# Kernel tuning notes

Hardware: AMD Instinct MI355X
Metric: run time of the kernel (lower is better)

Reference implementation:

```python
import jax, jax.numpy as jnp
import numpy as np

NUM_NODE = 100000
B, L, D = 128, 50, 128
HOP = 2
S = 8            # n_sample
NEIGHBOR_N = 9   # FindNeighbors top-k
BETA = 0.005
LEAKY = 0.2      # opt.alpha


def _local_agg(h, adj, a_local):
    # h: [B,N,D], adj: [B,N,N] int with edge types 0..4, a_local: [4,D]
    # e_k[b,i,j] = leakyrelu(sum_d h[b,i,d]*h[b,j,d]*a_k[d]) without [B,N,N,D] blowup
    e = jnp.stack([jnp.einsum('bid,bjd->bij', h * a_local[k], h) for k in range(4)])
    e = jax.nn.leaky_relu(e, LEAKY)
    att = jnp.full(e.shape[1:], -9e15, dtype=h.dtype)
    for k in range(4):
        att = jnp.where(adj == k + 1, e[k], att)
    att = jax.nn.softmax(att, axis=-1)
    return att @ h


def _global_agg(self_v, neigh_v, neigh_w, extra, w1, w2, w3):
    # self_v [B,M,D], neigh_v [B,M,S,D], neigh_w [B,M,S], extra (session info) [B,M,D]
    x = jnp.concatenate([extra[:, :, None, :] * neigh_v, neigh_w[..., None]], axis=-1)  # [B,M,S,D+1]
    alpha = jax.nn.leaky_relu(jnp.einsum('bmse,ed->bmsd', x, w1), LEAKY)
    alpha = jax.nn.softmax(jnp.einsum('bmsd,d->bms', alpha, w2[:, 0]), axis=-1)
    neigh = jnp.sum(alpha[..., None] * neigh_v, axis=-2)                                # [B,M,D]
    out = jnp.concatenate([self_v, neigh], axis=-1) @ w3
    return jax.nn.relu(out)


def _ssl(h_local, h_global):
    b, l, _ = h_local.shape
    kr, kc = jax.random.split(jax.random.key(42))
    corrupted = h_local[jax.random.permutation(kr, b)][:, jax.random.permutation(kc, l)]
    pos = jnp.sum(h_local * h_global, axis=1)
    neg = jnp.sum(h_global * corrupted, axis=1)
    return jnp.sum(-jnp.log(1e-8 + jax.nn.sigmoid(pos))
                   - jnp.log(1e-8 + 1.0 - jax.nn.sigmoid(neg)))


def _compute_scores(hidden, mask, pos_embedding, w1, w2, glu1_w, glu1_b, glu2_w, embedding):
    b, l, d = hidden.shape
    m = mask.astype(hidden.dtype)[..., None]                       # [B,L,1]
    pos = jnp.broadcast_to(pos_embedding[:l][None], hidden.shape)  # [B,L,D]
    hs = jnp.sum(hidden * m, axis=1) / jnp.sum(m, axis=1)          # [B,D]
    nh = jnp.tanh(jnp.concatenate([pos, hidden], axis=-1) @ w1)
    ns = jax.nn.sigmoid(nh @ glu1_w.T + glu1_b + hs[:, None, :] @ glu2_w.T)
    beta = (ns @ w2) * m                                           # [B,L,1]
    select = jnp.sum(beta * hidden, axis=1)                        # [B,D]
    # FindNeighbors: top-k cosine-similarity attention across the batch
    norm = jnp.sqrt(jnp.sum(select * select + 1e-6, axis=1))[:, None]
    cos = jax.nn.softmax((select @ select.T) / (norm @ norm.T), axis=-1)
    k = min(NEIGHBOR_N, b)
    topv, topi = jax.lax.top_k(cos, k)
    topv = jax.nn.softmax(topv, axis=-1)
    neighbor = jnp.sum(topv[..., None] * select[topi], axis=1)     # [B,D]
    select = select + neighbor                                     # dropout40: eval identity
    return select @ embedding[1:].T                                # [B, num_node-1]


def _forward(inputs, adj, mask_item, item, adj_all, num_w, embedding, pos_embedding,
             a_local, gw1, gw2, gw3, w1, w2, glu1_w, glu1_b, glu2_w):
    b, l = inputs.shape
    d = embedding.shape[1]
    h = embedding[inputs]
    h_local = _local_agg(h, adj, a_local)
    # multi-hop neighbor sampling via global adjacency table
    item_neighbors = [inputs]
    weight_neighbors = []
    support = l
    for _ in range(HOP):
        flat = item_neighbors[-1].reshape(-1)
        support *= S
        item_neighbors.append(adj_all[flat].reshape(b, support))
        weight_neighbors.append(num_w[flat].reshape(b, support))
    entity = [embedding[x] for x in item_neighbors]
    mf = mask_item.astype(h.dtype)
    item_emb = embedding[item] * mf[..., None]
    sess = jnp.sum(item_emb, axis=1) / jnp.sum(mf, axis=-1)[:, None]   # [B,D]
    session_info = [jnp.broadcast_to(sess[:, None, :], ev.shape) for ev in entity[:HOP]]
    for n_hop in range(HOP):
        nxt = []
        for i in range(HOP - n_hop):
            nv = entity[i + 1].reshape(b, -1, S, d)
            nw = weight_neighbors[i].reshape(b, -1, S)
            nxt.append(_global_agg(entity[i], nv, nw, session_info[i],
                                   gw1[n_hop], gw2[n_hop], gw3[n_hop]))
        entity = nxt
    h_global = entity[0].reshape(b, l, d)
    output = h_local + h_global  # dropout_local/global: eval identity
    con_loss = _ssl(h_local, h_global)
    scores = _compute_scores(output, mask_item, pos_embedding, w1, w2,
                             glu1_w, glu1_b, glu2_w, embedding)
    return output, BETA * con_loss, scores


def setup_inputs() -> dict:
    key = jax.random.key(0)
    ks = jax.random.split(key, 18)
    s = 0.08  # ~ uniform(-1/sqrt(D), 1/sqrt(D)) scale
    return {
        'inputs': jax.random.randint(ks[0], (B, L), 0, NUM_NODE, dtype=jnp.int32),
        'adj': jax.random.randint(ks[1], (B, L, L), 0, 5, dtype=jnp.int32),
        'mask_item': jax.random.randint(ks[2], (B, L), 0, 2, dtype=jnp.int32).at[:, 0].set(1),
        'item': jax.random.randint(ks[3], (B, L), 0, NUM_NODE, dtype=jnp.int32),
        'targets': jax.random.randint(ks[4], (B,), 0, NUM_NODE, dtype=jnp.int32),
        'adj_all': jax.random.randint(ks[5], (NUM_NODE, S), 0, NUM_NODE, dtype=jnp.int32),
        'num_w': jax.random.uniform(ks[6], (NUM_NODE, S), dtype=jnp.float32),
        'embedding': jax.random.normal(ks[7], (NUM_NODE, D), dtype=jnp.float32) * s,
        'pos_embedding': jax.random.normal(ks[8], (200, D), dtype=jnp.float32) * s,
        'a_local': jax.random.normal(ks[9], (4, D), dtype=jnp.float32) * s,
        'gw1': jax.random.normal(ks[10], (HOP, D + 1, D), dtype=jnp.float32) * s,
        'gw2': jax.random.normal(ks[11], (HOP, D, 1), dtype=jnp.float32) * s,
        'gw3': jax.random.normal(ks[12], (HOP, 2 * D, D), dtype=jnp.float32) * s,
        'w1': jax.random.normal(ks[13], (2 * D, D), dtype=jnp.float32) * s,
        'w2': jax.random.normal(ks[14], (D, 1), dtype=jnp.float32) * s,
        'glu1_w': jax.random.normal(ks[15], (D, D), dtype=jnp.float32) * s,
        'glu1_b': jax.random.normal(ks[16], (D,), dtype=jnp.float32) * s,
        'glu2_w': jax.random.normal(ks[17], (D, D), dtype=jnp.float32) * s,
    }


def reference(inputs, adj, mask_item, item, targets, adj_all, num_w, embedding,
              pos_embedding, a_local, gw1, gw2, gw3, w1, w2, glu1_w, glu1_b, glu2_w):
    # targets embedding lookup in the original is dead code (targets1 unused)
    return _forward(inputs, adj, mask_item, item, adj_all, num_w, embedding,
                    pos_embedding, a_local, gw1, gw2, gw3, w1, w2, glu1_w, glu1_b, glu2_w)
```

## Files before the change

kernel.cpp:

```cpp
#include <hip/hip_runtime.h>
#include <stdint.h>

namespace {
constexpr int B_ = 128;
constexpr int L_ = 50;
constexpr int D_ = 128;
constexpr int S_ = 8;
constexpr int NSC_ = 99999;
constexpr int NBR_ = 9;
}
#define LEAKY_ 0.2f
#define BETA_ 0.005f

typedef __attribute__((ext_vector_type(8))) __bf16 bf16x8;
typedef __attribute__((ext_vector_type(4))) float f32x4;

__device__ __forceinline__ float leaky_(float x){ return x >= 0.f ? x : LEAKY_*x; }
__device__ __forceinline__ float sigm_(float x){ return 1.f/(1.f+expf(-x)); }

__device__ __forceinline__ short f2b(float f){
  uint32_t u = __float_as_uint(f);
  u += 0x7fffu + ((u >> 16) & 1u);
  return (short)(u >> 16);
}
__device__ __forceinline__ float b2f(short s){
  return __uint_as_float(((uint32_t)(uint16_t)s) << 16);
}
__device__ __forceinline__ f32x4 zero4(){ f32x4 z = {0.f,0.f,0.f,0.f}; return z; }
__device__ __forceinline__ f32x4 mfma_bf16(bf16x8 a, bf16x8 b, f32x4 c){
  return __builtin_amdgcn_mfma_f32_16x16x32_bf16(a, b, c, 0, 0, 0);
}

__device__ __forceinline__ void tf2x32(uint32_t k0, uint32_t k1, uint32_t c0, uint32_t c1,
                                       uint32_t* o0, uint32_t* o1){
  uint32_t ks2 = k0 ^ k1 ^ 0x1BD11BDAu;
  uint32_t x0 = c0 + k0, x1 = c1 + k1;
#define RND_(r) { x0 += x1; x1 = (x1<<(r))|(x1>>(32-(r))); x1 ^= x0; }
  RND_(13) RND_(15) RND_(26) RND_(6)   x0 += k1;  x1 += ks2 + 1u;
  RND_(17) RND_(29) RND_(16) RND_(24)  x0 += ks2; x1 += k0  + 2u;
  RND_(13) RND_(15) RND_(26) RND_(6)   x0 += k0;  x1 += k1  + 3u;
  RND_(17) RND_(29) RND_(16) RND_(24)  x0 += k1;  x1 += ks2 + 4u;
  RND_(13) RND_(15) RND_(26) RND_(6)   x0 += ks2; x1 += k0  + 5u;
#undef RND_
  *o0 = x0; *o1 = x1;
}

__global__ __launch_bounds__(256) void k_prep_all(
    const float* __restrict__ emb, const int* __restrict__ item,
    const int* __restrict__ mask, const float* __restrict__ gw1,
    const float* __restrict__ gw3, const float* __restrict__ glu1w,
    const int* __restrict__ inputs, const int* __restrict__ adj_all,
    const float* __restrict__ num_w,
    short* __restrict__ embB, float* __restrict__ glu1wT,
    short* __restrict__ w3T,
    int* __restrict__ n1i, float* __restrict__ n1w,
    int* __restrict__ n2i, float* __restrict__ n2w,
    short* __restrict__ Bsess)
{
  int blk = blockIdx.x, tid = threadIdx.x;
  if (blk < 3125){
    size_t base = (size_t)blk*4096 + (size_t)tid*16;
    float4 f0 = *(const float4*)(emb + base);
    float4 f1 = *(const float4*)(emb + base + 4);
    float4 f2 = *(const float4*)(emb + base + 8);
    float4 f3 = *(const float4*)(emb + base + 12);
    short4 s0, s1, s2, s3;
    s0.x=f2b(f0.x); s0.y=f2b(f0.y); s0.z=f2b(f0.z); s0.w=f2b(f0.w);
    s1.x=f2b(f1.x); s1.y=f2b(f1.y); s1.z=f2b(f1.z); s1.w=f2b(f1.w);
    s2.x=f2b(f2.x); s2.y=f2b(f2.y); s2.z=f2b(f2.z); s2.w=f2b(f2.w);
    s3.x=f2b(f3.x); s3.y=f2b(f3.y); s3.z=f2b(f3.z); s3.w=f2b(f3.w);
    *(short4*)(embB + base)      = s0;
    *(short4*)(embB + base + 4)  = s1;
    *(short4*)(embB + base + 8)  = s2;
    *(short4*)(embB + base + 12) = s3;
  } else if (blk < 3445){
    int o = (blk - 3125)*256 + tid;
    if (o < 16384){
      int e = o >> 7, t = o & 127;
      glu1wT[o] = glu1w[t*128 + e];
    } else {
      int o3 = o - 16384;
      int hop = o3 >> 15, r = o3 & 32767;
      int nn = r >> 8, k = r & 255;
      w3T[hop*(128*264) + nn*264 + k] = f2b(gw3[hop*(256*128) + k*128 + nn]);
    }
  } else if (blk < 3645){
    int p = (blk - 3445)*256 + tid;
    int base = inputs[p >> 3];
    int off  = base*S_ + (p & 7);
    int i1 = adj_all[off];
    n1i[p] = i1;
    n1w[p] = num_w[off];
#pragma unroll
    for (int j = 0; j < 8; j++){
      n2i[(size_t)p*8 + j] = adj_all[i1*8 + j];
      n2w[(size_t)p*8 + j] = num_w[i1*8 + j];
    }
  } else {
    int i = blk - 3645;
    int hop = i >> 7, b = i & 127;
    __shared__ float sessS[128];
    if (tid < 128){
      float acc = 0.f, ms = 0.f;
      for (int l = 0; l < L_; l++){
        float mk = (float)mask[b*L_ + l];
        ms += mk;
        acc += mk * emb[(size_t)item[b*L_ + l]*D_ + tid];
      }
      sessS[tid] = acc / ms;
    }
    __syncthreads();
    const float* g1 = gw1 + hop*(129*128);
    short* outp = Bsess + ((size_t)hop*128 + b)*16384;
    for (int it = 0; it < 64; it++){
      int u = it*256 + tid;
      int e = u & 127, d = u >> 7;
      outp[u] = f2b(g1[e*128 + d] * sessS[e]);
    }
  }
}

__global__ __launch_bounds__(256, 4) void k_fused1(
    const short* __restrict__ embB, const int* __restrict__ inputs,
    const int* __restrict__ adj, const float* __restrict__ a_local,
    float* __restrict__ hl,
    const int* __restrict__ n1i, const float* __restrict__ n1w,
    const int* __restrict__ n2i, const float* __restrict__ n2w,
    const short* __restrict__ Bsess,
    const float* __restrict__ w1g, const float* __restrict__ w2g,
    short* __restrict__ e0pB, short* __restrict__ e1pB)
{
  __shared__ __align__(16) short As[128*136];
  __shared__ float w1lS[128], w2S[128], nwsS[128], logitsS[128], alphaS[128];
  const int blk = blockIdx.x;
  const int tid = threadIdx.x;

  if (blk < 256){
    float* hs   = (float*)As;
    float* attL = (float*)(As + 12900);
    float* al   = (float*)(As + 15500);
    int*   idxs = (int*)  (As + 16556);
    int b = blk >> 1, half = blk & 1;
    int i0 = half*25;
    if (tid < L_) idxs[tid] = inputs[b*L_ + tid];
    __syncthreads();
    for (int u = tid; u < L_*16; u += 256){
      int i = u >> 4, c = u & 15;
      union { bf16x8 v; short sh[8]; } w;
      w.v = *(const bf16x8*)&embB[(size_t)idxs[i]*128 + c*8];
#pragma unroll
      for (int j = 0; j < 8; j++) hs[i*129 + c*8 + j] = b2f(w.sh[j]);
    }
    for (int e = tid; e < 4*D_; e += 256) al[(e>>7)*132 + (e&127)] = a_local[e];
    __syncthreads();
    for (int p = tid; p < 25*L_; p += 256){
      int il = p / L_, j = p % L_;
      int i = i0 + il;
      int k = adj[((size_t)b*L_ + i)*L_ + j];
      float v = -9e15f;
      if (k >= 1){
        const float* ak = &al[(k-1)*132];
        float acc = 0.f;
        for (int d = 0; d < D_; d++) acc += hs[i*129+d]*hs[j*129+d]*ak[d];
        v = leaky_(acc);
      }
      attL[il*52 + j] = v;
    }
    __syncthreads();
    if (tid < 25){
      int il = tid;
      float mx = -INFINITY;
      for (int j = 0; j < L_; j++) mx = fmaxf(mx, attL[il*52+j]);
      float sm = 0.f;
      for (int j = 0; j < L_; j++){ float e_ = expf(attL[il*52+j] - mx); attL[il*52+j] = e_; sm += e_; }
      float inv = 1.f/sm;
      for (int j = 0; j < L_; j++) attL[il*52+j] *= inv;
    }
    __syncthreads();
    for (int q = tid; q < 25*D_; q += 256){
      int il = q >> 7, d = q & 127;
      float acc = 0.f;
      for (int j = 0; j < L_; j++) acc += attL[il*52+j]*hs[j*129+d];
      hl[((size_t)b*L_ + i0 + il)*D_ + d] = acc;
    }
    return;
  }

  int b, r0, rpb;
  const int* nidx; const float* nw; short* outn;
  if (blk < 768){
    int i = blk - 256;
    b = i >> 2; r0 = (i & 3)*128;
    nidx = n1i; nw = n1w; outn = e0pB; rpb = 400;
  } else {
    int i = blk - 768;
    b = i / 25; r0 = (i % 25)*128;
    nidx = n2i; nw = n2w; outn = e1pB; rpb = 3200;
  }
  if (tid < 128){
    w1lS[tid]  = w1g[128*128 + tid];
    w2S[tid]   = w2g[tid];
    int rr = min(r0 + tid, rpb - 1);
    nwsS[tid]  = nw[(size_t)b*rpb + rr];
  }
  for (int it = 0; it < 8; it++){
    int u = it*256 + tid;
    int lr = u >> 4, c = u & 15;
    int rr = min(r0 + lr, rpb - 1);
    const short* src = embB + (size_t)nidx[(size_t)b*rpb + rr]*128;
    *(bf16x8*)&As[lr*136 + c*8] = *(const bf16x8*)&src[c*8];
  }
  __syncthreads();
  const int lane = tid & 63, wave = tid >> 6;
  const int quad = lane >> 4, l16 = lane & 15;
  const int wr0 = wave * 32;
  const short* Bb = Bsess + (size_t)b*16384;
  f32x4 acc[2][8];
#pragma unroll
  for (int i=0;i<2;i++)
#pragma unroll
    for (int j=0;j<8;j++) acc[i][j] = zero4();
  for (int kc = 0; kc < 4; kc++){
    int k = kc*32 + quad*8;
    bf16x8 a0 = *(const bf16x8*)&As[(wr0 + l16)*136 + k];
    bf16x8 a1 = *(const bf16x8*)&As[(wr0 + 16 + l16)*136 + k];
    bf16x8 bb[8];
#pragma unroll
    for (int nt = 0; nt < 8; nt++)
      bb[nt] = *(const bf16x8*)&Bb[(size_t)(nt*16 + l16)*128 + k];
#pragma unroll
    for (int nt = 0; nt < 8; nt++){
      acc[0][nt] = mfma_bf16(a0, bb[nt], acc[0][nt]);
      acc[1][nt] = mfma_bf16(a1, bb[nt], acc[1][nt]);
    }
  }
#pragma unroll
  for (int rt = 0; rt < 2; rt++){
#pragma unroll
    for (int r = 0; r < 4; r++){
      int rowl = wr0 + rt*16 + quad*4 + r;
      float nwv = nwsS[rowl];
      float c = 0.f;
#pragma unroll
      for (int nt = 0; nt < 8; nt++){
        int col = nt*16 + l16;
        float v = acc[rt][nt][r] + nwv * w1lS[col];
        c += leaky_(v) * w2S[col];
      }
      c += __shfl_xor(c, 1, 64);
      c += __shfl_xor(c, 2, 64);
      c += __shfl_xor(c, 4, 64);
      c += __shfl_xor(c, 8, 64);
      if (l16 == 0) logitsS[rowl] = c;
    }
  }
  __syncthreads();
  if (tid < 16){
    float mx = -INFINITY;
    for (int s = 0; s < 8; s++) mx = fmaxf(mx, logitsS[tid*8+s]);
    float sm = 0.f; float ev[8];
    for (int s = 0; s < 8; s++){ ev[s] = expf(logitsS[tid*8+s]-mx); sm += ev[s]; }
    for (int s = 0; s < 8; s++) alphaS[tid*8+s] = ev[s]/sm;
  }
  __syncthreads();
  {
    int mg = tid >> 4;
    int dc = tid & 15;
    float o[8];
#pragma unroll
    for (int j = 0; j < 8; j++) o[j] = 0.f;
#pragma unroll
    for (int s = 0; s < 8; s++){
      float al2 = alphaS[mg*8+s];
      union { bf16x8 v; short sh[8]; } u;
      u.v = *(const bf16x8*)&As[(mg*8+s)*136 + dc*8];
#pragma unroll
      for (int j = 0; j < 8; j++) o[j] += al2 * b2f(u.sh[j]);
    }
    if (r0 + mg*8 < rpb){
      int m = (r0 >> 3) + mg;
      union { short s[8]; bf16x8 v; } pk;
#pragma unroll
      for (int j = 0; j < 8; j++) pk.s[j] = f2b(o[j]);
      *(bf16x8*)(outn + ((size_t)b*(rpb>>3) + m)*128 + dc*8) = pk.v;
    }
  }
}

__global__ __launch_bounds__(256, 4) void k_att(
    const short* __restrict__ embB, const short* __restrict__ denseB,
    const int* __restrict__ nidx, const float* __restrict__ nw,
    const short* __restrict__ Bsess,
    const float* __restrict__ w1g, const float* __restrict__ w2g,
    short* __restrict__ outn, int rpb)
{
  __shared__ __align__(16) short As[128*136];
  __shared__ float w1lS[128], w2S[128], nwsS[128], logitsS[128], alphaS[128];
  const int tid = threadIdx.x;
  const int b = blockIdx.y;
  const int r0 = blockIdx.x * 128;
  if (tid < 128){
    w1lS[tid]  = w1g[128*128 + tid];
    w2S[tid]   = w2g[tid];
    int rr = min(r0 + tid, rpb - 1);
    nwsS[tid]  = nw[(size_t)b*rpb + rr];
  }
  for (int it = 0; it < 8; it++){
    int u = it*256 + tid;
    int lr = u >> 4, c = u & 15;
    int rr = min(r0 + lr, rpb - 1);
    const short* src = denseB ? denseB + ((size_t)b*rpb + rr)*128
                              : embB + (size_t)nidx[(size_t)b*rpb + rr]*128;
    *(bf16x8*)&As[lr*136 + c*8] = *(const bf16x8*)&src[c*8];
  }
  __syncthreads();
  const int lane = tid & 63, wave = tid >> 6;
  const int quad = lane >> 4, l16 = lane & 15;
  const int wr0 = wave * 32;
  const short* Bb = Bsess + (size_t)b*16384;
  f32x4 acc[2][8];
#pragma unroll
  for (int i=0;i<2;i++)
#pragma unroll
    for (int j=0;j<8;j++) acc[i][j] = zero4();
  for (int kc = 0; kc < 4; kc++){
    int k = kc*32 + quad*8;
    bf16x8 a0 = *(const bf16x8*)&As[(wr0 + l16)*136 + k];
    bf16x8 a1 = *(const bf16x8*)&As[(wr0 + 16 + l16)*136 + k];
    bf16x8 bb[8];
#pragma unroll
    for (int nt = 0; nt < 8; nt++)
      bb[nt] = *(const bf16x8*)&Bb[(size_t)(nt*16 + l16)*128 + k];
#pragma unroll
    for (int nt = 0; nt < 8; nt++){
      acc[0][nt] = mfma_bf16(a0, bb[nt], acc[0][nt]);
      acc[1][nt] = mfma_bf16(a1, bb[nt], acc[1][nt]);
    }
  }
#pragma unroll
  for (int rt = 0; rt < 2; rt++){
#pragma unroll
    for (int r = 0; r < 4; r++){
      int rowl = wr0 + rt*16 + quad*4 + r;
      float nwv = nwsS[rowl];
      float c = 0.f;
#pragma unroll
      for (int nt = 0; nt < 8; nt++){
        int col = nt*16 + l16;
        float v = acc[rt][nt][r] + nwv * w1lS[col];
        c += leaky_(v) * w2S[col];
      }
      c += __shfl_xor(c, 1, 64);
      c += __shfl_xor(c, 2, 64);
      c += __shfl_xor(c, 4, 64);
      c += __shfl_xor(c, 8, 64);
      if (l16 == 0) logitsS[rowl] = c;
    }
  }
  __syncthreads();
  if (tid < 16){
    float mx = -INFINITY;
    for (int s = 0; s < 8; s++) mx = fmaxf(mx, logitsS[tid*8+s]);
    float sm = 0.f; float ev[8];
    for (int s = 0; s < 8; s++){ ev[s] = expf(logitsS[tid*8+s]-mx); sm += ev[s]; }
    for (int s = 0; s < 8; s++) alphaS[tid*8+s] = ev[s]/sm;
  }
  __syncthreads();
  {
    int mg = tid >> 4;
    int dc = tid & 15;
    float o[8];
#pragma unroll
    for (int j = 0; j < 8; j++) o[j] = 0.f;
#pragma unroll
    for (int s = 0; s < 8; s++){
      float al = alphaS[mg*8+s];
      union { bf16x8 v; short sh[8]; } u;
      u.v = *(const bf16x8*)&As[(mg*8+s)*136 + dc*8];
#pragma unroll
      for (int j = 0; j < 8; j++) o[j] += al * b2f(u.sh[j]);
    }
    if (r0 + mg*8 < rpb){
      int m = (r0 >> 3) + mg;
      union { short s[8]; bf16x8 v; } pk;
#pragma unroll
      for (int j = 0; j < 8; j++) pk.s[j] = f2b(o[j]);
      *(bf16x8*)(outn + ((size_t)b*(rpb>>3) + m)*128 + dc*8) = pk.v;
    }
  }
}

__global__ __launch_bounds__(256) void k_gout2(
    const short* __restrict__ embB, const int* __restrict__ inputs,
    const int* __restrict__ n1i, const short* __restrict__ w3T,
    short* __restrict__ e0pB, short* __restrict__ e1pB)
{
  const int blk = blockIdx.x;
  const int* self_idx; short* buf; int rblk;
  if (blk < 100){ self_idx = inputs; buf = e0pB; rblk = blk; }
  else          { self_idx = n1i;    buf = e1pB; rblk = blk - 100; }
  const int tid = threadIdx.x;
  const int lane = tid & 63, wave = tid >> 6;
  const int quad = lane >> 4, l16 = lane & 15;
  const int rbase = rblk*64 + wave*16;
  const int row = rbase + l16;
  const short* selfp = embB + (size_t)self_idx[row]*128;
  const short* neighp = buf + (size_t)row*128;
  f32x4 acc[8];
#pragma unroll
  for (int i=0;i<8;i++) acc[i] = zero4();
  for (int kc = 0; kc < 4; kc++){
    int k = kc*32 + quad*8;
    bf16x8 a = *(const bf16x8*)&selfp[k];
#pragma unroll
    for (int nt = 0; nt < 8; nt++){
      bf16x8 bb = *(const bf16x8*)&w3T[(size_t)(nt*16 + l16)*264 + k];
      acc[nt] = mfma_bf16(a, bb, acc[nt]);
    }
  }
  for (int kc = 4; kc < 8; kc++){
    int k = kc*32 + quad*8;
    bf16x8 a = *(const bf16x8*)&neighp[k - 128];
#pragma unroll
    for (int nt = 0; nt < 8; nt++){
      bf16x8 bb = *(const bf16x8*)&w3T[(size_t)(nt*16 + l16)*264 + k];
      acc[nt] = mfma_bf16(a, bb, acc[nt]);
    }
  }
#pragma unroll
  for (int nt = 0; nt < 8; nt++)
#pragma unroll
    for (int r = 0; r < 4; r++){
      int orow = rbase + quad*4 + r;
      buf[(size_t)orow*128 + nt*16 + l16] = f2b(fmaxf(acc[nt][r], 0.f));
    }
}

__global__ __launch_bounds__(256) void k_gout(
    const short* __restrict__ embB, const short* __restrict__ selfB,
    const int* __restrict__ self_idx, const short* __restrict__ w3T,
    const short* __restrict__ neighB, float* __restrict__ outF,
    short* __restrict__ outB)
{
  const int tid = threadIdx.x;
  const int lane = tid & 63, wave = tid >> 6;
  const int quad = lane >> 4, l16 = lane & 15;
  const int rbase = blockIdx.x*64 + wave*16;
  const int row = rbase + l16;
  const short* selfp = self_idx ? embB + (size_t)self_idx[row]*128
                                : selfB + (size_t)row*128;
  const short* neighp = neighB + (size_t)row*128;
  f32x4 acc[8];
#pragma unroll
  for (int i=0;i<8;i++) acc[i] = zero4();
  for (int kc = 0; kc < 4; kc++){
    int k = kc*32 + quad*8;
    bf16x8 a = *(const bf16x8*)&selfp[k];
#pragma unroll
    for (int nt = 0; nt < 8; nt++){
      bf16x8 bb = *(const bf16x8*)&w3T[(size_t)(nt*16 + l16)*264 + k];
      acc[nt] = mfma_bf16(a, bb, acc[nt]);
    }
  }
  for (int kc = 4; kc < 8; kc++){
    int k = kc*32 + quad*8;
    bf16x8 a = *(const bf16x8*)&neighp[k - 128];
#pragma unroll
    for (int nt = 0; nt < 8; nt++){
      bf16x8 bb = *(const bf16x8*)&w3T[(size_t)(nt*16 + l16)*264 + k];
      acc[nt] = mfma_bf16(a, bb, acc[nt]);
    }
  }
  if (outF){
#pragma unroll
    for (int nt = 0; nt < 8; nt++)
#pragma unroll
      for (int r = 0; r < 4; r++){
        int orow = rbase + quad*4 + r;
        outF[(size_t)orow*128 + nt*16 + l16] = fmaxf(acc[nt][r], 0.f);
      }
  } else {
#pragma unroll
    for (int nt = 0; nt < 8; nt++)
#pragma unroll
      for (int r = 0; r < 4; r++){
        int orow = rbase + quad*4 + r;
        outB[(size_t)orow*128 + nt*16 + l16] = f2b(fmaxf(acc[nt][r], 0.f));
      }
  }
}

__global__ __launch_bounds__(128) void k_sslhs(
    const float* __restrict__ hl, const float* __restrict__ hg,
    const int* __restrict__ mask, const float* __restrict__ glu2_w,
    float* __restrict__ out, float* __restrict__ wsLoss,
    float* __restrict__ g2)
{
  __shared__ uint32_t keys[128];
  __shared__ float red[128];
  __shared__ float hss[128];
  __shared__ int pcS[50];
  __shared__ int prbS;
  int b = blockIdx.x, tid = threadIdx.x;
  uint32_t kr0, kr1, kc0, kc1, sk0, sk1, o0, o1;
  tf2x32(0u, 42u, 0u, 0u, &kr0, &kr1);
  tf2x32(0u, 42u, 0u, 1u, &kc0, &kc1);
  tf2x32(kr0, kr1, 0u, 1u, &sk0, &sk1);
  tf2x32(sk0, sk1, 0u, (uint32_t)tid, &o0, &o1);
  keys[tid] = o0 ^ o1;
  __syncthreads();
  {
    uint32_t mk = keys[tid];
    int rank = 0;
    for (int j = 0; j < 128; j++){
      uint32_t kj = keys[j];
      rank += (kj < mk) || (kj == mk && j < tid);
    }
    if (rank == b) prbS = tid;
  }
  __syncthreads();
  tf2x32(kc0, kc1, 0u, 1u, &sk0, &sk1);
  if (tid < 50){
    tf2x32(sk0, sk1, 0u, (uint32_t)tid, &o0, &o1);
    keys[tid] = o0 ^ o1;
  }
  __syncthreads();
  if (tid < 50){
    uint32_t mk = keys[tid];
    int rank = 0;
    for (int j = 0; j < 50; j++){
      uint32_t kj = keys[j];
      rank += (kj < mk) || (kj == mk && j < tid);
    }
    pcS[rank] = tid;
  }
  __syncthreads();
  int prb = prbS, d = tid;
  float pos = 0.f, neg = 0.f, hsacc = 0.f, ms = 0.f;
  for (int l = 0; l < L_; l++){
    size_t off = ((size_t)b*L_ + l)*D_ + d;
    float hlv = hl[off], hgv = hg[off];
    float o = hlv + hgv;
    out[off] = o;
    pos += hlv * hgv;
    neg += hgv * hl[((size_t)prb*L_ + pcS[l])*D_ + d];
    float mk = (float)mask[b*L_ + l];
    ms += mk;
    hsacc += mk * o;
  }
  hss[d] = hsacc / ms;
  red[d] = -logf(1e-8f + sigm_(pos)) - logf(1e-8f + 1.f - sigm_(neg));
  __syncthreads();
  for (int off = 64; off >= 1; off >>= 1){
    if (d < off) red[d] += red[d + off];
    __syncthreads();
  }
  if (d == 0) wsLoss[b] = red[0];
  float g = 0.f;
  for (int e = 0; e < 128; e++) g += hss[e]*glu2_w[d*128 + e];
  g2[(size_t)b*128 + d] = g;
}

__global__ __launch_bounds__(256) void k_beta10(
    const float* __restrict__ hidden, const int* __restrict__ mask,
    const float* __restrict__ pose, const float* __restrict__ w1s,
    const float* __restrict__ w2s, const float* __restrict__ glu1wT,
    const float* __restrict__ glu1b, const float* __restrict__ g2,
    float* __restrict__ betaW)
{
  __shared__ float x[10][260];
  __shared__ float buf[10][132];
  __shared__ float bufB[2][16];
  int lg = blockIdx.x, b = blockIdx.y, tid = threadIdx.x;
  int t = tid & 127, eh = tid >> 7;
  int l0 = lg*10;
  for (int u = tid; u < 10*64; u += 256){
    int row = u >> 6, c4 = u & 63;
    float4 v; int col;
    if (c4 < 32){ v = *(const float4*)(pose + (l0+row)*128 + c4*4); col = c4*4; }
    else        { v = *(const float4*)(hidden + ((size_t)b*L_ + l0+row)*128 + (c4-32)*4); col = 128 + (c4-32)*4; }
    *(float4*)&x[row][col] = v;
  }
  __syncthreads();
  float acc[10];
#pragma unroll
  for (int l = 0; l < 10; l++) acc[l] = 0.f;
  {
    int e0 = eh*128;
    for (int e = e0; e < e0 + 128; e += 4){
      float wa = w1s[(e+0)*128 + t];
      float wb = w1s[(e+1)*128 + t];
      float wc = w1s[(e+2)*128 + t];
      float wd = w1s[(e+3)*128 + t];
#pragma unroll
      for (int l = 0; l < 10; l++){
        float4 xv = *(const float4*)&x[l][e];
        acc[l] += xv.x*wa; acc[l] += xv.y*wb; acc[l] += xv.z*wc; acc[l] += xv.w*wd;
      }
    }
  }
  if (eh == 1){
#pragma unroll
    for (int i = 0; i < 10; i++) buf[i][t] = acc[i];
  }
  __syncthreads();
  if (eh == 0){
#pragma unroll
    for (int i = 0; i < 10; i++) acc[i] += buf[i][t];
  }
  __syncthreads();
  if (eh == 0){
#pragma unroll
    for (int l = 0; l < 10; l++) x[l][t] = tanhf(acc[l]);
  }
  __syncthreads();
  float acc2[10];
#pragma unroll
  for (int l = 0; l < 10; l++) acc2[l] = 0.f;
  {
    int e0 = eh*64;
    for (int e = e0; e < e0 + 64; e += 4){
      float wa = glu1wT[(e+0)*128 + t];
      float wb = glu1wT[(e+1)*128 + t];
      float wc = glu1wT[(e+2)*128 + t];
      float wd = glu1wT[(e+3)*128 + t];
#pragma unroll
      for (int l = 0; l < 10; l++){
        float4 xv = *(const float4*)&x[l][e];
        acc2[l] += xv.x*wa; acc2[l] += xv.y*wb; acc2[l] += xv.z*wc; acc2[l] += xv.w*wd;
      }
    }
  }
  if (eh == 1){
#pragma unroll
    for (int i = 0; i < 10; i++) buf[i][t] = acc2[i];
  }
  __syncthreads();
  if (eh == 0){
#pragma unroll
    for (int i = 0; i < 10; i++) acc2[i] += buf[i][t];
  }
  __syncthreads();
  if (eh == 0){
    float g2v = g2[(size_t)b*128 + t];
    float g1b = glu1b[t];
    float w2v = w2s[t];
    int lane = tid & 63, wv = tid >> 6;
#pragma unroll
    for (int l = 0; l < 10; l++){
      float ns = sigm_(acc2[l] + g1b + g2v);
      float v = ns * w2v;
      v += __shfl_xor(v, 1, 64);
      v += __shfl_xor(v, 2, 64);
      v += __shfl_xor(v, 4, 64);
      v += __shfl_xor(v, 8, 64);
      v += __shfl_xor(v, 16, 64);
      v += __shfl_xor(v, 32, 64);
      if (lane == 0) bufB[wv][l] = v;
    }
  }
  __syncthreads();
  if (tid < 10)
    betaW[b*L_ + l0 + tid] = (bufB[0][tid] + bufB[1][tid]) * (float)mask[b*L_ + l0 + tid];
}

__global__ __launch_bounds__(128) void k_selnorm(
    const float* __restrict__ hidden, const float* __restrict__ betaW,
    float* __restrict__ select, float* __restrict__ norms)
{
  __shared__ float bet[56];
  __shared__ float red[128];
  int b = blockIdx.x, t = threadIdx.x;
  if (t < L_) bet[t] = betaW[b*L_ + t];
  __syncthreads();
  float sel = 0.f;
  for (int l = 0; l < L_; l++) sel += bet[l]*hidden[((size_t)b*L_ + l)*128 + t];
  select[(size_t)b*128 + t] = sel;
  red[t] = sel*sel + 1e-6f;
  __syncthreads();
  for (int off=64; off>=1; off>>=1){ if (t<off) red[t]+=red[t+off]; __syncthreads(); }
  if (t==0) norms[b] = sqrtf(red[0]);
}

__global__ __launch_bounds__(128) void k_topk(const float* __restrict__ select,
                                              const float* __restrict__ norms,
                                              const float* __restrict__ wsLoss,
                                              short* __restrict__ select2b,
                                              float* __restrict__ out_loss){
  __shared__ float p[B_];
  __shared__ float red[128];
  __shared__ float tv[NBR_];
  __shared__ int   ti[NBR_];
  int b = blockIdx.x, t = threadIdx.x;
  float dot = 0.f;
  for (int d = 0; d < D_; d++) dot += select[(size_t)b*D_ + d]*select[(size_t)t*D_ + d];
  float logit = dot / (norms[b]*norms[t]);
  red[t] = logit; __syncthreads();
  for (int off = 64; off >= 1; off >>= 1){
    if (t < off) red[t] = fmaxf(red[t], red[t + off]);
    __syncthreads();
  }
  float mx = red[0]; __syncthreads();
  float e_ = expf(logit - mx);
  red[t] = e_; __syncthreads();
  for (int off = 64; off >= 1; off >>= 1){
    if (t < off) red[t] += red[t + off];
    __syncthreads();
  }
  p[t] = e_ / red[0];
  __syncthreads();
  if (t == 0){
    unsigned long long used0 = 0ull, used1 = 0ull;
    for (int k = 0; k < NBR_; k++){
      float best = -INFINITY; int bi = 0;
      for (int j = 0; j < B_; j++){
        bool u = (j < 64) ? ((used0 >> j) & 1ull) : ((used1 >> (j-64)) & 1ull);
        if (!u && p[j] > best){ best = p[j]; bi = j; }
      }
      if (bi < 64) used0 |= 1ull << bi; else used1 |= 1ull << (bi-64);
      tv[k] = best; ti[k] = bi;
    }
    float mx2 = -INFINITY;
    for (int k = 0; k < NBR_; k++) mx2 = fmaxf(mx2, tv[k]);
    float s2 = 0.f;
    for (int k = 0; k < NBR_; k++){ tv[k] = expf(tv[k]-mx2); s2 += tv[k]; }
    for (int k = 0; k < NBR_; k++) tv[k] /= s2;
  }
  __syncthreads();
  float nb = 0.f;
#pragma unroll
  for (int k = 0; k < NBR_; k++) nb += tv[k]*select[(size_t)ti[k]*D_ + t];
  select2b[(size_t)b*D_ + t] = f2b(select[(size_t)b*D_ + t] + nb);
  if (b == 0){
    __syncthreads();
    red[t] = wsLoss[t];
    __syncthreads();
    for (int off = 64; off >= 1; off >>= 1){
      if (t < off) red[t] += red[t + off];
      __syncthreads();
    }
    if (t == 0) out_loss[0] = BETA_ * red[0];
  }
}

__global__ __launch_bounds__(256) void k_scores(
    const short* __restrict__ sel2b, const float* __restrict__ emb,
    float* __restrict__ scores)
{
  __shared__ __align__(16) short Es[64*136];
  const int tid = threadIdx.x;
  const int n0 = blockIdx.x*64;
  for (int it = 0; it < 8; it++){
    int u = it*256 + tid;
    int lr = u >> 5, c = u & 31;
    int n = min(n0 + lr, NSC_ - 1);
    float4 v = *(const float4*)(emb + (size_t)(1 + n)*128 + c*4);
    short4 s4; s4.x=f2b(v.x); s4.y=f2b(v.y); s4.z=f2b(v.z); s4.w=f2b(v.w);
    *(short4*)&Es[lr*136 + c*4] = s4;
  }
  __syncthreads();
  const int lane = tid & 63, wave = tid >> 6;
  const int quad = lane >> 4, l16 = lane & 15;
  int n = n0 + wave*16 + l16;
  f32x4 acc[8];
#pragma unroll
  for (int i=0;i<8;i++) acc[i] = zero4();
  for (int kc = 0; kc < 4; kc++){
    int k = kc*32 + quad*8;
    bf16x8 bb = *(const bf16x8*)&Es[(wave*16 + l16)*136 + k];
#pragma unroll
    for (int rt = 0; rt < 8; rt++){
      bf16x8 a = *(const bf16x8*)&sel2b[(rt*16 + l16)*128 + k];
      acc[rt] = mfma_bf16(a, bb, acc[rt]);
    }
  }
  if (n < NSC_){
#pragma unroll
    for (int rt = 0; rt < 8; rt++)
#pragma unroll
      for (int r = 0; r < 4; r++){
        int brow = rt*16 + quad*4 + r;
        scores[(size_t)brow*NSC_ + n] = acc[rt][r];
      }
  }
}

extern "C" void kernel_launch(void* const* d_in, const int* in_sizes, int n_in,
                              void* d_out, int out_size, void* d_ws, size_t ws_size,
                              hipStream_t stream) {
  (void)in_sizes; (void)n_in; (void)out_size; (void)ws_size;
  const int*   inputs  = (const int*)  d_in[0];
  const int*   adj     = (const int*)  d_in[1];
  const int*   mask    = (const int*)  d_in[2];
  const int*   item    = (const int*)  d_in[3];
  const int*   adj_all = (const int*)  d_in[5];
  const float* num_w   = (const float*)d_in[6];
  const float* emb     = (const float*)d_in[7];
  const float* pose    = (const float*)d_in[8];
  const float* a_local = (const float*)d_in[9];
  const float* gw1     = (const float*)d_in[10];
  const float* gw2     = (const float*)d_in[11];
  const float* gw3     = (const float*)d_in[12];
  const float* w1      = (const float*)d_in[13];
  const float* w2      = (const float*)d_in[14];
  const float* glu1w   = (const float*)d_in[15];
  const float* glu1b   = (const float*)d_in[16];
  const float* glu2w   = (const float*)d_in[17];
  float* out = (float*)d_out;

  float* W     = (float*)d_ws;
  float* hl    = W;
  float* hg    = W + 819200;
  short* e0pB  = (short*)(W + 1638400);
  short* e1pB  = (short*)(W + 2457600);
  float* g2    = W + 9027584;
  float* sel   = W + 9043968;
  short* sel2b = (short*)(W + 9060352);
  float* norms = W + 9076736;
  float* wsLoss= W + 9076864;
  float* n1w   = W + 9076992;
  float* n2w   = W + 9128192;
  float* betaW = W + 9537792;
  float* glu1wT= W + 9576960;
  short* w3Tb  = (short*)(W + 9593344);
  int*   n1i   = (int*)(W + 9627136);
  int*   n2i   = n1i + 51200;

  short* embB   = (short*)(out + 819712);
  short* BsessG = (short*)(out + 819712 + 3200000);
  short* hgB    = (short*)(out + 819712 + 3200000 + 2097152);

  k_prep_all<<<3901, 256, 0, stream>>>(emb, item, mask, gw1, gw3, glu1w,
                                       inputs, adj_all, num_w,
                                       embB, glu1wT, w3Tb,
                                       n1i, n1w, n2i, n2w, BsessG);

  k_fused1<<<3968, 256, 0, stream>>>(embB, inputs, adj, a_local, hl,
                                     n1i, n1w, n2i, n2w, BsessG,
                                     gw1, gw2, e0pB, e1pB);
  k_gout2<<<900, 256, 0, stream>>>(embB, inputs, n1i, w3Tb, e0pB, e1pB);

  k_att <<<dim3(4, B_),  256, 0, stream>>>(embB, e1pB, nullptr, n1w,
                                           BsessG + (size_t)128*16384,
                                           gw1 + 129*128, gw2 + 128, hgB, 400);
  k_gout<<<100, 256, 0, stream>>>(embB, e0pB, nullptr, w3Tb + 128*264, hgB, hg, nullptr);

  k_sslhs<<<B_, 128, 0, stream>>>(hl, hg, mask, glu2w, out, wsLoss, g2);
  k_beta10<<<dim3(5, B_), 256, 0, stream>>>(out, mask, pose, w1, w2, glu1wT,
                                            glu1b, g2, betaW);
  k_selnorm<<<B_, 128, 0, stream>>>(out, betaW, sel, norms);
  k_topk<<<B_, 128, 0, stream>>>(sel, norms, wsLoss, sel2b, out + B_*L_*D_);
  k_scores<<<(NSC_ + 63)/64, 256, 0, stream>>>(sel2b, emb, out + B_*L_*D_ + 1);
}
```

Before: 450.4 us.

## Fuse hop-2 attention with output GEMM and fold select/norm into neighbors

```diff
diff --git a/kernel.cpp b/kernel.cpp
--- a/kernel.cpp
+++ b/kernel.cpp
@@ -287,109 +287,6 @@
   }
 }
 
-__global__ __launch_bounds__(256, 4) void k_att(
-    const short* __restrict__ embB, const short* __restrict__ denseB,
-    const int* __restrict__ nidx, const float* __restrict__ nw,
-    const short* __restrict__ Bsess,
-    const float* __restrict__ w1g, const float* __restrict__ w2g,
-    short* __restrict__ outn, int rpb)
-{
-  __shared__ __align__(16) short As[128*136];
-  __shared__ float w1lS[128], w2S[128], nwsS[128], logitsS[128], alphaS[128];
-  const int tid = threadIdx.x;
-  const int b = blockIdx.y;
-  const int r0 = blockIdx.x * 128;
-  if (tid < 128){
-    w1lS[tid]  = w1g[128*128 + tid];
-    w2S[tid]   = w2g[tid];
-    int rr = min(r0 + tid, rpb - 1);
-    nwsS[tid]  = nw[(size_t)b*rpb + rr];
-  }
-  for (int it = 0; it < 8; it++){
-    int u = it*256 + tid;
-    int lr = u >> 4, c = u & 15;
-    int rr = min(r0 + lr, rpb - 1);
-    const short* src = denseB ? denseB + ((size_t)b*rpb + rr)*128
-                              : embB + (size_t)nidx[(size_t)b*rpb + rr]*128;
-    *(bf16x8*)&As[lr*136 + c*8] = *(const bf16x8*)&src[c*8];
-  }
-  __syncthreads();
-  const int lane = tid & 63, wave = tid >> 6;
-  const int quad = lane >> 4, l16 = lane & 15;
-  const int wr0 = wave * 32;
-  const short* Bb = Bsess + (size_t)b*16384;
-  f32x4 acc[2][8];
-#pragma unroll
-  for (int i=0;i<2;i++)
-#pragma unroll
-    for (int j=0;j<8;j++) acc[i][j] = zero4();
-  for (int kc = 0; kc < 4; kc++){
-    int k = kc*32 + quad*8;
-    bf16x8 a0 = *(const bf16x8*)&As[(wr0 + l16)*136 + k];
-    bf16x8 a1 = *(const bf16x8*)&As[(wr0 + 16 + l16)*136 + k];
-    bf16x8 bb[8];
-#pragma unroll
-    for (int nt = 0; nt < 8; nt++)
-      bb[nt] = *(const bf16x8*)&Bb[(size_t)(nt*16 + l16)*128 + k];
-#pragma unroll
-    for (int nt = 0; nt < 8; nt++){
-      acc[0][nt] = mfma_bf16(a0, bb[nt], acc[0][nt]);
-      acc[1][nt] = mfma_bf16(a1, bb[nt], acc[1][nt]);
-    }
-  }
-#pragma unroll
-  for (int rt = 0; rt < 2; rt++){
-#pragma unroll
-    for (int r = 0; r < 4; r++){
-      int rowl = wr0 + rt*16 + quad*4 + r;
-      float nwv = nwsS[rowl];
-      float c = 0.f;
-#pragma unroll
-      for (int nt = 0; nt < 8; nt++){
-        int col = nt*16 + l16;
-        float v = acc[rt][nt][r] + nwv * w1lS[col];
-        c += leaky_(v) * w2S[col];
-      }
-      c += __shfl_xor(c, 1, 64);
-      c += __shfl_xor(c, 2, 64);
-      c += __shfl_xor(c, 4, 64);
-      c += __shfl_xor(c, 8, 64);
-      if (l16 == 0) logitsS[rowl] = c;
-    }
-  }
-  __syncthreads();
-  if (tid < 16){
-    float mx = -INFINITY;
-    for (int s = 0; s < 8; s++) mx = fmaxf(mx, logitsS[tid*8+s]);
-    float sm = 0.f; float ev[8];
-    for (int s = 0; s < 8; s++){ ev[s] = expf(logitsS[tid*8+s]-mx); sm += ev[s]; }
-    for (int s = 0; s < 8; s++) alphaS[tid*8+s] = ev[s]/sm;
-  }
-  __syncthreads();
-  {
-    int mg = tid >> 4;
-    int dc = tid & 15;
-    float o[8];
-#pragma unroll
-    for (int j = 0; j < 8; j++) o[j] = 0.f;
-#pragma unroll
-    for (int s = 0; s < 8; s++){
-      float al = alphaS[mg*8+s];
-      union { bf16x8 v; short sh[8]; } u;
-      u.v = *(const bf16x8*)&As[(mg*8+s)*136 + dc*8];
-#pragma unroll
-      for (int j = 0; j < 8; j++) o[j] += al * b2f(u.sh[j]);
-    }
-    if (r0 + mg*8 < rpb){
-      int m = (r0 >> 3) + mg;
-      union { short s[8]; bf16x8 v; } pk;
-#pragma unroll
-      for (int j = 0; j < 8; j++) pk.s[j] = f2b(o[j]);
-      *(bf16x8*)(outn + ((size_t)b*(rpb>>3) + m)*128 + dc*8) = pk.v;
-    }
-  }
-}
-
 __global__ __launch_bounds__(256) void k_gout2(
     const short* __restrict__ embB, const int* __restrict__ inputs,
     const int* __restrict__ n1i, const short* __restrict__ w3T,
@@ -436,57 +333,132 @@
     }
 }
 
-__global__ __launch_bounds__(256) void k_gout(
-    const short* __restrict__ embB, const short* __restrict__ selfB,
-    const int* __restrict__ self_idx, const short* __restrict__ w3T,
-    const short* __restrict__ neighB, float* __restrict__ outF,
-    short* __restrict__ outB)
+__global__ __launch_bounds__(256) void k_attg1(
+    const short* __restrict__ e1pB, const short* __restrict__ e0pB,
+    const float* __restrict__ n1w, const short* __restrict__ Bsess,
+    const float* __restrict__ w1g, const float* __restrict__ w2g,
+    const short* __restrict__ w3T, float* __restrict__ hg)
 {
+  __shared__ __align__(16) short As[128*136];
+  __shared__ __align__(16) short GA[16*264];
+  __shared__ float w1lS[128], w2S[128], nwsS[128], logitsS[128], alphaS[128];
   const int tid = threadIdx.x;
+  const int b = blockIdx.y;
+  const int r0 = blockIdx.x * 128;
+  const int rpb = 400, mpb = 50;
+  const int m0 = r0 >> 3;
+  if (tid < 128){
+    w1lS[tid]  = w1g[128*128 + tid];
+    w2S[tid]   = w2g[tid];
+    int rr = min(r0 + tid, rpb - 1);
+    nwsS[tid]  = n1w[(size_t)b*rpb + rr];
+  }
+  for (int it = 0; it < 8; it++){
+    int u = it*256 + tid;
+    int lr = u >> 4, c = u & 15;
+    int rr = min(r0 + lr, rpb - 1);
+    *(bf16x8*)&As[lr*136 + c*8] =
+      *(const bf16x8*)&e1pB[((size_t)b*rpb + rr)*128 + c*8];
+  }
+  {
+    int r = tid >> 4, c = tid & 15;
+    int g = b*mpb + min(m0 + r, mpb - 1);
+    *(bf16x8*)&GA[r*264 + c*8] = *(const bf16x8*)&e0pB[(size_t)g*128 + c*8];
+  }
+  __syncthreads();
   const int lane = tid & 63, wave = tid >> 6;
   const int quad = lane >> 4, l16 = lane & 15;
-  const int rbase = blockIdx.x*64 + wave*16;
-  const int row = rbase + l16;
-  const short* selfp = self_idx ? embB + (size_t)self_idx[row]*128
-                                : selfB + (size_t)row*128;
-  const short* neighp = neighB + (size_t)row*128;
-  f32x4 acc[8];
-#pragma unroll
-  for (int i=0;i<8;i++) acc[i] = zero4();
+  const int wr0 = wave * 32;
+  const short* Bb = Bsess + (size_t)b*16384;
+  f32x4 acc[2][8];
+#pragma unroll
+  for (int i=0;i<2;i++)
+#pragma unroll
+    for (int j=0;j<8;j++) acc[i][j] = zero4();
   for (int kc = 0; kc < 4; kc++){
     int k = kc*32 + quad*8;
-    bf16x8 a = *(const bf16x8*)&selfp[k];
+    bf16x8 a0 = *(const bf16x8*)&As[(wr0 + l16)*136 + k];
+    bf16x8 a1 = *(const bf16x8*)&As[(wr0 + 16 + l16)*136 + k];
+    bf16x8 bb[8];
+#pragma unroll
+    for (int nt = 0; nt < 8; nt++)
+      bb[nt] = *(const bf16x8*)&Bb[(size_t)(nt*16 + l16)*128 + k];
 #pragma unroll
     for (int nt = 0; nt < 8; nt++){
+      acc[0][nt] = mfma_bf16(a0, bb[nt], acc[0][nt]);
+      acc[1][nt] = mfma_bf16(a1, bb[nt], acc[1][nt]);
+    }
+  }
+#pragma unroll
+  for (int rt = 0; rt < 2; rt++){
+#pragma unroll
+    for (int r = 0; r < 4; r++){
+      int rowl = wr0 + rt*16 + quad*4 + r;
+      float nwv = nwsS[rowl];
+      float c = 0.f;
+#pragma unroll
+      for (int nt = 0; nt < 8; nt++){
+        int col = nt*16 + l16;
+        float v = acc[rt][nt][r] + nwv * w1lS[col];
+        c += leaky_(v) * w2S[col];
+      }
+      c += __shfl_xor(c, 1, 64);
+      c += __shfl_xor(c, 2, 64);
+      c += __shfl_xor(c, 4, 64);
+      c += __shfl_xor(c, 8, 64);
+      if (l16 == 0) logitsS[rowl] = c;
+    }
+  }
+  __syncthreads();
+  if (tid < 16){
+    float mx = -INFINITY;
+    for (int s = 0; s < 8; s++) mx = fmaxf(mx, logitsS[tid*8+s]);
+    float sm = 0.f; float ev[8];
+    for (int s = 0; s < 8; s++){ ev[s] = expf(logitsS[tid*8+s]-mx); sm += ev[s]; }
+    for (int s = 0; s < 8; s++) alphaS[tid*8+s] = ev[s]/sm;
+  }
+  __syncthreads();
+  {
+    int mg = tid >> 4;
+    int dc = tid & 15;
+    float o[8];
+#pragma unroll
+    for (int j = 0; j < 8; j++) o[j] = 0.f;
+#pragma unroll
+    for (int s = 0; s < 8; s++){
+      float al2 = alphaS[mg*8+s];
+      union { bf16x8 v; short sh[8]; } u;
+      u.v = *(const bf16x8*)&As[(mg*8+s)*136 + dc*8];
+#pragma unroll
+      for (int j = 0; j < 8; j++) o[j] += al2 * b2f(u.sh[j]);
+    }
+    union { short s[8]; bf16x8 v; } pk;
+#pragma unroll
+    for (int j = 0; j < 8; j++) pk.s[j] = f2b(o[j]);
+    *(bf16x8*)&GA[mg*264 + 128 + dc*8] = pk.v;
+  }
+  __syncthreads();
+  f32x4 gacc[2];
+  gacc[0] = zero4(); gacc[1] = zero4();
+  for (int kc = 0; kc < 8; kc++){
+    int k = kc*32 + quad*8;
+    bf16x8 a = *(const bf16x8*)&GA[l16*264 + k];
+#pragma unroll
+    for (int j = 0; j < 2; j++){
+      int nt = wave*2 + j;
       bf16x8 bb = *(const bf16x8*)&w3T[(size_t)(nt*16 + l16)*264 + k];
-      acc[nt] = mfma_bf16(a, bb, acc[nt]);
-    }
-  }
-  for (int kc = 4; kc < 8; kc++){
-    int k = kc*32 + quad*8;
-    bf16x8 a = *(const bf16x8*)&neighp[k - 128];
-#pragma unroll
-    for (int nt = 0; nt < 8; nt++){
-      bf16x8 bb = *(const bf16x8*)&w3T[(size_t)(nt*16 + l16)*264 + k];
-      acc[nt] = mfma_bf16(a, bb, acc[nt]);
-    }
-  }
-  if (outF){
-#pragma unroll
-    for (int nt = 0; nt < 8; nt++)
-#pragma unroll
-      for (int r = 0; r < 4; r++){
-        int orow = rbase + quad*4 + r;
-        outF[(size_t)orow*128 + nt*16 + l16] = fmaxf(acc[nt][r], 0.f);
-      }
-  } else {
-#pragma unroll
-    for (int nt = 0; nt < 8; nt++)
-#pragma unroll
-      for (int r = 0; r < 4; r++){
-        int orow = rbase + quad*4 + r;
-        outB[(size_t)orow*128 + nt*16 + l16] = f2b(fmaxf(acc[nt][r], 0.f));
-      }
+      gacc[j] = mfma_bf16(a, bb, gacc[j]);
+    }
+  }
+#pragma unroll
+  for (int j = 0; j < 2; j++){
+    int col = (wave*2 + j)*16 + l16;
+#pragma unroll
+    for (int r = 0; r < 4; r++){
+      int ml = m0 + quad*4 + r;
+      if (ml < mpb)
+        hg[((size_t)b*mpb + ml)*128 + col] = fmaxf(gacc[j][r], 0.f);
+    }
   }
 }
 
@@ -494,7 +466,7 @@
     const float* __restrict__ hl, const float* __restrict__ hg,
     const int* __restrict__ mask, const float* __restrict__ glu2_w,
     float* __restrict__ out, float* __restrict__ wsLoss,
-    float* __restrict__ g2)
+    float* __restrict__ g2, float* __restrict__ select)
 {
   __shared__ uint32_t keys[128];
   __shared__ float red[128];
@@ -502,6 +474,7 @@
   __shared__ int pcS[50];
   __shared__ int prbS;
   int b = blockIdx.x, tid = threadIdx.x;
+  select[(size_t)b*128 + tid] = 0.f;
   uint32_t kr0, kr1, kc0, kc1, sk0, sk1, o0, o1;
   tf2x32(0u, 42u, 0u, 0u, &kr0, &kr1);
   tf2x32(0u, 42u, 0u, 1u, &kc0, &kc1);
@@ -566,11 +539,12 @@
     const float* __restrict__ pose, const float* __restrict__ w1s,
     const float* __restrict__ w2s, const float* __restrict__ glu1wT,
     const float* __restrict__ glu1b, const float* __restrict__ g2,
-    float* __restrict__ betaW)
+    float* __restrict__ select)
 {
   __shared__ float x[10][260];
   __shared__ float buf[10][132];
   __shared__ float bufB[2][16];
+  __shared__ float bet10[10];
   int lg = blockIdx.x, b = blockIdx.y, tid = threadIdx.x;
   int t = tid & 127, eh = tid >> 7;
   int l0 = lg*10;
@@ -661,40 +635,35 @@
   }
   __syncthreads();
   if (tid < 10)
-    betaW[b*L_ + l0 + tid] = (bufB[0][tid] + bufB[1][tid]) * (float)mask[b*L_ + l0 + tid];
-}
-
-__global__ __launch_bounds__(128) void k_selnorm(
-    const float* __restrict__ hidden, const float* __restrict__ betaW,
-    float* __restrict__ select, float* __restrict__ norms)
-{
-  __shared__ float bet[56];
-  __shared__ float red[128];
-  int b = blockIdx.x, t = threadIdx.x;
-  if (t < L_) bet[t] = betaW[b*L_ + t];
-  __syncthreads();
-  float sel = 0.f;
-  for (int l = 0; l < L_; l++) sel += bet[l]*hidden[((size_t)b*L_ + l)*128 + t];
-  select[(size_t)b*128 + t] = sel;
-  red[t] = sel*sel + 1e-6f;
-  __syncthreads();
-  for (int off=64; off>=1; off>>=1){ if (t<off) red[t]+=red[t+off]; __syncthreads(); }
-  if (t==0) norms[b] = sqrtf(red[0]);
+    bet10[tid] = (bufB[0][tid] + bufB[1][tid]) * (float)mask[b*L_ + l0 + tid];
+  __syncthreads();
+  if (eh == 0){
+    float part = 0.f;
+#pragma unroll
+    for (int i = 0; i < 10; i++) part += bet10[i] * x[i][128 + t];
+    atomicAdd(&select[(size_t)b*128 + t], part);
+  }
 }
 
 __global__ __launch_bounds__(128) void k_topk(const float* __restrict__ select,
-                                              const float* __restrict__ norms,
                                               const float* __restrict__ wsLoss,
                                               short* __restrict__ select2b,
                                               float* __restrict__ out_loss){
   __shared__ float p[B_];
   __shared__ float red[128];
+  __shared__ float nrm[128];
   __shared__ float tv[NBR_];
   __shared__ int   ti[NBR_];
   int b = blockIdx.x, t = threadIdx.x;
-  float dot = 0.f;
-  for (int d = 0; d < D_; d++) dot += select[(size_t)b*D_ + d]*select[(size_t)t*D_ + d];
-  float logit = dot / (norms[b]*norms[t]);
+  float dot = 0.f, nsq = 0.f;
+  for (int d = 0; d < D_; d++){
+    float sv = select[(size_t)t*D_ + d];
+    dot += select[(size_t)b*D_ + d]*sv;
+    nsq += sv*sv + 1e-6f;
+  }
+  nrm[t] = sqrtf(nsq);
+  __syncthreads();
+  float logit = dot / (nrm[b]*nrm[t]);
   red[t] = logit; __syncthreads();
   for (int off = 64; off >= 1; off >>= 1){
     if (t < off) red[t] = fmaxf(red[t], red[t + off]);
@@ -816,11 +785,9 @@
   float* g2    = W + 9027584;
   float* sel   = W + 9043968;
   short* sel2b = (short*)(W + 9060352);
-  float* norms = W + 9076736;
   float* wsLoss= W + 9076864;
   float* n1w   = W + 9076992;
   float* n2w   = W + 9128192;
-  float* betaW = W + 9537792;
   float* glu1wT= W + 9576960;
   short* w3Tb  = (short*)(W + 9593344);
   int*   n1i   = (int*)(W + 9627136);
@@ -828,7 +795,6 @@
 
   short* embB   = (short*)(out + 819712);
   short* BsessG = (short*)(out + 819712 + 3200000);
-  short* hgB    = (short*)(out + 819712 + 3200000 + 2097152);
 
   k_prep_all<<<3901, 256, 0, stream>>>(emb, item, mask, gw1, gw3, glu1w,
                                        inputs, adj_all, num_w,
@@ -840,15 +806,14 @@
                                      gw1, gw2, e0pB, e1pB);
   k_gout2<<<900, 256, 0, stream>>>(embB, inputs, n1i, w3Tb, e0pB, e1pB);
 
-  k_att <<<dim3(4, B_),  256, 0, stream>>>(embB, e1pB, nullptr, n1w,
+  k_attg1<<<dim3(4, B_), 256, 0, stream>>>(e1pB, e0pB, n1w,
                                            BsessG + (size_t)128*16384,
-                                           gw1 + 129*128, gw2 + 128, hgB, 400);
-  k_gout<<<100, 256, 0, stream>>>(embB, e0pB, nullptr, w3Tb + 128*264, hgB, hg, nullptr);
-
-  k_sslhs<<<B_, 128, 0, stream>>>(hl, hg, mask, glu2w, out, wsLoss, g2);
+                                           gw1 + 129*128, gw2 + 128,
+                                           w3Tb + 128*264, hg);
+
+  k_sslhs<<<B_, 128, 0, stream>>>(hl, hg, mask, glu2w, out, wsLoss, g2, sel);
   k_beta10<<<dim3(5, B_), 256, 0, stream>>>(out, mask, pose, w1, w2, glu1wT,
-                                            glu1b, g2, betaW);
-  k_selnorm<<<B_, 128, 0, stream>>>(out, betaW, sel, norms);
-  k_topk<<<B_, 128, 0, stream>>>(sel, norms, wsLoss, sel2b, out + B_*L_*D_);
+                                            glu1b, g2, sel);
+  k_topk<<<B_, 128, 0, stream>>>(sel, wsLoss, sel2b, out + B_*L_*D_);
   k_scores<<<(NSC_ + 63)/64, 256, 0, stream>>>(sel2b, emb, out + B_*L_*D_ + 1);
 }
```

After: 444.0 us. Within noise of the previous version (-1.4%).
